# Kernel tuning notes

Hardware: AMD Instinct MI355X
Metric: run time of the kernel (lower is better)

## Reference

```python
import jax, jax.numpy as jnp
import numpy as np

N = 1_000_000   # total points across batch
INC = 128       # channel width (inc)
B = 16          # number of scans in batch
HID = INC // 4  # reduction=4


def setup_inputs() -> dict:
    key = jax.random.key(0)
    k1, k2, k3, k4 = jax.random.split(key, 4)
    feats = jax.random.normal(k1, (N, INC), dtype=jnp.float32)
    batch_idx = jnp.sort(jax.random.randint(k2, (N,), 0, B, dtype=jnp.int32))
    W1 = jax.random.normal(k3, (INC, HID), dtype=jnp.float32) * 0.05
    b1 = jnp.zeros((HID,), dtype=jnp.float32)
    W2 = jax.random.normal(k4, (HID, INC), dtype=jnp.float32) * 0.05
    b2 = jnp.zeros((INC,), dtype=jnp.float32)
    return {"feats": feats, "batch_idx": batch_idx, "W1": W1, "b1": b1, "W2": W2, "b2": b2}


def reference(feats, batch_idx, W1, b1, W2, b2):
    # Segment (per-scan) mean and max over points -> [B, INC].
    counts = jax.ops.segment_sum(jnp.ones((feats.shape[0],), feats.dtype), batch_idx, num_segments=B)
    seg_sum = jax.ops.segment_sum(feats, batch_idx, num_segments=B)
    seg_mean = seg_sum / jnp.maximum(counts, 1.0)[:, None]
    seg_max = jax.ops.segment_max(feats, batch_idx, num_segments=B)
    seg_max = jnp.where(counts[:, None] > 0, seg_max, 0.0)  # guard empty segments

    def mlp(z):
        return jax.nn.relu(z @ W1 + b1) @ W2 + b2

    # sigmoid(MLP(avg) + MLP(max)); pooled values are identical for every
    # point of a segment, so apply MLP on [B, INC] and gather per point.
    gate = jax.nn.sigmoid(mlp(seg_mean) + mlp(seg_max))  # [B, INC]
    return feats * gate[batch_idx]                        # [N, INC]
```

## Files before the change

kernel.cpp:

```cpp
#include <hip/hip_runtime.h>
#include <math.h>

#define INC   128
#define HID   32
#define NSEG  16

typedef float f4v __attribute__((ext_vector_type(4)));

__device__ __forceinline__ float4 ntload4(const float4* p) {
    f4v v = __builtin_nontemporal_load((const f4v*)p);
    return make_float4(v.x, v.y, v.z, v.w);
}
__device__ __forceinline__ void ntstore4(float4* p, float4 f) {
    f4v v = {f.x, f.y, f.z, f.w};
    __builtin_nontemporal_store(v, (f4v*)p);
}

__device__ __forceinline__ unsigned f2ord(float f) {
    unsigned u = __float_as_uint(f);
    return (u & 0x80000000u) ? ~u : (u | 0x80000000u);
}
__device__ __forceinline__ float ord2f(unsigned u) {
    return (u & 0x80000000u) ? __uint_as_float(u & 0x7fffffffu)
                             : __uint_as_float(~u);
}

__device__ __forceinline__ void flush_lds8(int seg, int c8,
                                           const float4& s0, const float4& s1,
                                           const float4& m0, const float4& m1,
                                           float cnt, float* s_sum,
                                           unsigned* s_max, float* s_cnt) {
    int base = seg * INC + c8 * 8;
    atomicAdd(&s_sum[base + 0], s0.x);
    atomicAdd(&s_sum[base + 1], s0.y);
    atomicAdd(&s_sum[base + 2], s0.z);
    atomicAdd(&s_sum[base + 3], s0.w);
    atomicAdd(&s_sum[base + 4], s1.x);
    atomicAdd(&s_sum[base + 5], s1.y);
    atomicAdd(&s_sum[base + 6], s1.z);
    atomicAdd(&s_sum[base + 7], s1.w);
    atomicMax(&s_max[base + 0], f2ord(m0.x));
    atomicMax(&s_max[base + 1], f2ord(m0.y));
    atomicMax(&s_max[base + 2], f2ord(m0.z));
    atomicMax(&s_max[base + 3], f2ord(m0.w));
    atomicMax(&s_max[base + 4], f2ord(m1.x));
    atomicMax(&s_max[base + 5], f2ord(m1.y));
    atomicMax(&s_max[base + 6], f2ord(m1.z));
    atomicMax(&s_max[base + 7], f2ord(m1.w));
    if (c8 == 0) atomicAdd(&s_cnt[seg], cnt);
}

__global__ __launch_bounds__(256) void seg_reduce_kernel(
    const float4* __restrict__ feats4, const int* __restrict__ bidx,
    float* __restrict__ gsum, unsigned* __restrict__ gmax,
    float* __restrict__ gcnt, int nrows)
{
    __shared__ float    s_sum[NSEG * INC];
    __shared__ unsigned s_max[NSEG * INC];
    __shared__ float    s_cnt[NSEG];

    const int tid   = threadIdx.x;
    const int chunk = (nrows + gridDim.x - 1) / gridDim.x;
    const int start = blockIdx.x * chunk;
    if (start >= nrows) return;
    const int end = min(start + chunk, nrows);

    for (int i = tid; i < NSEG * INC; i += 256) { s_sum[i] = 0.f; s_max[i] = 0u; }
    if (tid < NSEG) s_cnt[tid] = 0.f;
    __syncthreads();

    const int c8   = tid & 15;
    const int slot = tid >> 4;
    int    cur = -1;
    float4 s0 = make_float4(0.f, 0.f, 0.f, 0.f), s1 = s0;
    float4 m0 = s0, m1 = s0;
    float  cnt = 0.f;

    for (int r = start + slot; r < end; r += 16) {
        int           seg  = bidx[r];
        const float4* rowp = feats4 + (size_t)r * (INC / 4) + c8 * 2;
        float4        f0   = ntload4(rowp);
        float4        f1   = ntload4(rowp + 1);
        if (seg != cur) {
            if (cur >= 0) flush_lds8(cur, c8, s0, s1, m0, m1, cnt, s_sum, s_max, s_cnt);
            cur = seg; s0 = f0; s1 = f1; m0 = f0; m1 = f1; cnt = 1.f;
        } else {
            s0.x += f0.x; s0.y += f0.y; s0.z += f0.z; s0.w += f0.w;
            s1.x += f1.x; s1.y += f1.y; s1.z += f1.z; s1.w += f1.w;
            m0.x = fmaxf(m0.x, f0.x); m0.y = fmaxf(m0.y, f0.y);
            m0.z = fmaxf(m0.z, f0.z); m0.w = fmaxf(m0.w, f0.w);
            m1.x = fmaxf(m1.x, f1.x); m1.y = fmaxf(m1.y, f1.y);
            m1.z = fmaxf(m1.z, f1.z); m1.w = fmaxf(m1.w, f1.w);
            cnt += 1.f;
        }
    }
    if (cur >= 0) flush_lds8(cur, c8, s0, s1, m0, m1, cnt, s_sum, s_max, s_cnt);
    __syncthreads();

    const int sf  = bidx[start];
    const int sl  = bidx[end - 1];
    const int col = tid & (INC - 1);
    for (int s = sf + (tid >> 7); s <= sl; s += 2) {
        atomicAdd(&gsum[s * INC + col], s_sum[s * INC + col]);
        atomicMax(&gmax[s * INC + col], s_max[s * INC + col]);
        if (col == 0) atomicAdd(&gcnt[s], s_cnt[s]);
    }
}

__global__ __launch_bounds__(256) void mlp_kernel(
    const float* __restrict__ gsum, const unsigned* __restrict__ gmax,
    const float* __restrict__ gcnt,
    const float* __restrict__ W1, const float* __restrict__ b1,
    const float* __restrict__ W2, const float* __restrict__ b2,
    float* __restrict__ gate)
{
    __shared__ float s_mean[NSEG * INC];
    __shared__ float s_max [NSEG * INC];
    __shared__ float s_h   [NSEG * HID];
    __shared__ float s_W1  [INC * HID];
    __shared__ float s_W2  [HID * INC];
    __shared__ float s_b1  [HID];
    __shared__ float s_b2  [INC];
    const int tid = threadIdx.x;

    for (int i = tid; i < INC * HID; i += 256) { s_W1[i] = W1[i]; s_W2[i] = W2[i]; }
    if (tid < HID) s_b1[tid] = b1[tid];
    if (tid < INC) s_b2[tid] = b2[tid];

    for (int i = tid; i < NSEG * INC; i += 256) {
        int   s = i >> 7;
        float c = gcnt[s];
        s_mean[i] = gsum[i] / fmaxf(c, 1.f);
        s_max[i]  = (c > 0.f) ? ord2f(gmax[i]) : 0.f;
    }
    __syncthreads();

    for (int i = tid; i < NSEG * HID; i += 256) {
        int s = i / HID, h = i % HID;
        float am = s_b1[h], ax = s_b1[h];
        for (int c = 0; c < INC; c++) {
            float w = s_W1[c * HID + h];
            am += s_mean[s * INC + c] * w;
            ax += s_max [s * INC + c] * w;
        }
        s_h[i] = fmaxf(am, 0.f) + fmaxf(ax, 0.f);
    }
    __syncthreads();

    for (int i = tid; i < NSEG * INC; i += 256) {
        int s = i >> 7, c = i & (INC - 1);
        float a = 2.f * s_b2[c];
        for (int h = 0; h < HID; h++) a += s_h[s * HID + h] * s_W2[h * INC + c];
        gate[i] = 1.f / (1.f + expf(-a));
    }
}

__global__ __launch_bounds__(256) void apply_kernel(
    const float4* __restrict__ feats4, const int* __restrict__ bidx,
    const float4* __restrict__ gate4, float4* __restrict__ out4, int nrows)
{
    __shared__ float4 s_gate[NSEG * (INC / 4)];
    for (int i = threadIdx.x; i < NSEG * (INC / 4); i += blockDim.x)
        s_gate[i] = gate4[i];
    __syncthreads();

    const int total = nrows * (INC / 4);
    for (int idx = blockIdx.x * blockDim.x + threadIdx.x; idx < total;
         idx += gridDim.x * blockDim.x) {
        int    r   = idx >> 5;
        int    c4  = idx & 31;
        int    seg = bidx[r];
        float4 f   = ntload4(&feats4[idx]);
        float4 g   = s_gate[seg * (INC / 4) + c4];
        ntstore4(&out4[idx],
                 make_float4(f.x * g.x, f.y * g.y, f.z * g.z, f.w * g.w));
    }
}

extern "C" void kernel_launch(void* const* d_in, const int* in_sizes, int n_in,
                              void* d_out, int out_size, void* d_ws, size_t ws_size,
                              hipStream_t stream) {
    const float* feats = (const float*)d_in[0];
    const int*   bidx  = (const int*)d_in[1];
    const float* W1    = (const float*)d_in[2];
    const float* b1    = (const float*)d_in[3];
    const float* W2    = (const float*)d_in[4];
    const float* b2    = (const float*)d_in[5];
    float*       out   = (float*)d_out;
    const int nrows    = in_sizes[1];

    char*     ws   = (char*)d_ws;
    float*    gsum = (float*)(ws);
    unsigned* gmax = (unsigned*)(ws + 8192);
    float*    gcnt = (float*)(ws + 16384);
    float*    gate = (float*)(ws + 16448);

    hipMemsetAsync(d_ws, 0, 16448, stream);

    seg_reduce_kernel<<<2048, 256, 0, stream>>>(
        (const float4*)feats, bidx, gsum, gmax, gcnt, nrows);
    mlp_kernel<<<1, 256, 0, stream>>>(gsum, gmax, gcnt, W1, b1, W2, b2, gate);
    apply_kernel<<<8192, 256, 0, stream>>>(
        (const float4*)feats, bidx, (const float4*)gate, (float4*)out, nrows);
}
```

Baseline: 926.5 us.

## Process segments in groups so reduce and apply reuse feats from cache

Splits the work into four groups of four segments. Each group runs a reduce kernel and then an apply kernel that computes its own gates, so the apply pass rereads a feats slice (about 128MB) that may still sit in the large last-level cache. Nontemporal loads are dropped so the data can stay cached. The separate MLP kernel is folded into each apply block, which recomputes the gate MLP redundantly from global weights. The cost is eight launches instead of three, binary searches, and per-block MLP overhead.

```diff
diff --git a/kernel.cpp b/kernel.cpp
--- a/kernel.cpp
+++ b/kernel.cpp
@@ -1,16 +1,14 @@
 #include <hip/hip_runtime.h>
 #include <math.h>
 
-#define INC   128
-#define HID   32
-#define NSEG  16
+#define INC    128
+#define HID    32
+#define NSEG   16
+#define SPG    4
+#define NGRP   (NSEG / SPG)
+#define NBLK   2048
 
 typedef float f4v __attribute__((ext_vector_type(4)));
-
-__device__ __forceinline__ float4 ntload4(const float4* p) {
-    f4v v = __builtin_nontemporal_load((const f4v*)p);
-    return make_float4(v.x, v.y, v.z, v.w);
-}
 __device__ __forceinline__ void ntstore4(float4* p, float4 f) {
     f4v v = {f.x, f.y, f.z, f.w};
     __builtin_nontemporal_store(v, (f4v*)p);
@@ -25,49 +23,51 @@
                              : __uint_as_float(~u);
 }
 
-__device__ __forceinline__ void flush_lds8(int seg, int c8,
+__device__ __forceinline__ int lower_bound(const int* __restrict__ a, int n, int v) {
+    int lo = 0, hi = n;
+    while (lo < hi) { int m = (lo + hi) >> 1; if (a[m] < v) lo = m + 1; else hi = m; }
+    return lo;
+}
+
+__device__ __forceinline__ void flush_lds8(int sseg, int c8,
                                            const float4& s0, const float4& s1,
                                            const float4& m0, const float4& m1,
                                            float cnt, float* s_sum,
                                            unsigned* s_max, float* s_cnt) {
-    int base = seg * INC + c8 * 8;
-    atomicAdd(&s_sum[base + 0], s0.x);
-    atomicAdd(&s_sum[base + 1], s0.y);
-    atomicAdd(&s_sum[base + 2], s0.z);
-    atomicAdd(&s_sum[base + 3], s0.w);
-    atomicAdd(&s_sum[base + 4], s1.x);
-    atomicAdd(&s_sum[base + 5], s1.y);
-    atomicAdd(&s_sum[base + 6], s1.z);
-    atomicAdd(&s_sum[base + 7], s1.w);
-    atomicMax(&s_max[base + 0], f2ord(m0.x));
-    atomicMax(&s_max[base + 1], f2ord(m0.y));
-    atomicMax(&s_max[base + 2], f2ord(m0.z));
-    atomicMax(&s_max[base + 3], f2ord(m0.w));
-    atomicMax(&s_max[base + 4], f2ord(m1.x));
-    atomicMax(&s_max[base + 5], f2ord(m1.y));
-    atomicMax(&s_max[base + 6], f2ord(m1.z));
-    atomicMax(&s_max[base + 7], f2ord(m1.w));
-    if (c8 == 0) atomicAdd(&s_cnt[seg], cnt);
+    int base = sseg * INC + c8 * 8;
+    atomicAdd(&s_sum[base + 0], s0.x);  atomicAdd(&s_sum[base + 1], s0.y);
+    atomicAdd(&s_sum[base + 2], s0.z);  atomicAdd(&s_sum[base + 3], s0.w);
+    atomicAdd(&s_sum[base + 4], s1.x);  atomicAdd(&s_sum[base + 5], s1.y);
+    atomicAdd(&s_sum[base + 6], s1.z);  atomicAdd(&s_sum[base + 7], s1.w);
+    atomicMax(&s_max[base + 0], f2ord(m0.x));  atomicMax(&s_max[base + 1], f2ord(m0.y));
+    atomicMax(&s_max[base + 2], f2ord(m0.z));  atomicMax(&s_max[base + 3], f2ord(m0.w));
+    atomicMax(&s_max[base + 4], f2ord(m1.x));  atomicMax(&s_max[base + 5], f2ord(m1.y));
+    atomicMax(&s_max[base + 6], f2ord(m1.z));  atomicMax(&s_max[base + 7], f2ord(m1.w));
+    if (c8 == 0) atomicAdd(&s_cnt[sseg], cnt);
 }
 
-__global__ __launch_bounds__(256) void seg_reduce_kernel(
+__global__ __launch_bounds__(256) void seg_reduce_group(
     const float4* __restrict__ feats4, const int* __restrict__ bidx,
     float* __restrict__ gsum, unsigned* __restrict__ gmax,
-    float* __restrict__ gcnt, int nrows)
+    float* __restrict__ gcnt, int nrows, int seg_lo)
 {
-    __shared__ float    s_sum[NSEG * INC];
-    __shared__ unsigned s_max[NSEG * INC];
-    __shared__ float    s_cnt[NSEG];
+    __shared__ float    s_sum[SPG * INC];
+    __shared__ unsigned s_max[SPG * INC];
+    __shared__ float    s_cnt[SPG];
+    __shared__ int      s_bounds[2];
 
-    const int tid   = threadIdx.x;
-    const int chunk = (nrows + gridDim.x - 1) / gridDim.x;
-    const int start = blockIdx.x * chunk;
-    if (start >= nrows) return;
-    const int end = min(start + chunk, nrows);
+    const int tid = threadIdx.x;
+    if (tid < 2) s_bounds[tid] = lower_bound(bidx, nrows, seg_lo + tid * SPG);
+    for (int i = tid; i < SPG * INC; i += 256) { s_sum[i] = 0.f; s_max[i] = 0u; }
+    if (tid < SPG) s_cnt[tid] = 0.f;
+    __syncthreads();
 
-    for (int i = tid; i < NSEG * INC; i += 256) { s_sum[i] = 0.f; s_max[i] = 0u; }
-    if (tid < NSEG) s_cnt[tid] = 0.f;
-    __syncthreads();
+    const int r0 = s_bounds[0], r1 = s_bounds[1];
+    if (r1 <= r0) return;
+    const int chunk = (r1 - r0 + NBLK - 1) / NBLK;
+    const int rs = min(r0 + (int)blockIdx.x * chunk, r1);
+    const int re = min(rs + chunk, r1);
+    if (rs >= re) return;
 
     const int c8   = tid & 15;
     const int slot = tid >> 4;
@@ -76,13 +76,14 @@
     float4 m0 = s0, m1 = s0;
     float  cnt = 0.f;
 
-    for (int r = start + slot; r < end; r += 16) {
+    for (int r = rs + slot; r < re; r += 16) {
         int           seg  = bidx[r];
-        const float4* rowp = feats4 + (size_t)r * (INC / 4) + c8 * 2;
-        float4        f0   = ntload4(rowp);
-        float4        f1   = ntload4(rowp + 1);
+        const float4* rowp = feats4 + (size_t)r * 32 + c8 * 2;
+        float4        f0   = rowp[0];
+        float4        f1   = rowp[1];
         if (seg != cur) {
-            if (cur >= 0) flush_lds8(cur, c8, s0, s1, m0, m1, cnt, s_sum, s_max, s_cnt);
+            if (cur >= 0) flush_lds8(cur - seg_lo, c8, s0, s1, m0, m1, cnt,
+                                     s_sum, s_max, s_cnt);
             cur = seg; s0 = f0; s1 = f1; m0 = f0; m1 = f1; cnt = 1.f;
         } else {
             s0.x += f0.x; s0.y += f0.y; s0.z += f0.z; s0.w += f0.w;
@@ -94,85 +95,76 @@
             cnt += 1.f;
         }
     }
-    if (cur >= 0) flush_lds8(cur, c8, s0, s1, m0, m1, cnt, s_sum, s_max, s_cnt);
+    if (cur >= 0) flush_lds8(cur - seg_lo, c8, s0, s1, m0, m1, cnt,
+                             s_sum, s_max, s_cnt);
     __syncthreads();
 
-    const int sf  = bidx[start];
-    const int sl  = bidx[end - 1];
+    const int sf  = bidx[rs] - seg_lo;
+    const int sl  = bidx[re - 1] - seg_lo;
     const int col = tid & (INC - 1);
     for (int s = sf + (tid >> 7); s <= sl; s += 2) {
-        atomicAdd(&gsum[s * INC + col], s_sum[s * INC + col]);
-        atomicMax(&gmax[s * INC + col], s_max[s * INC + col]);
-        if (col == 0) atomicAdd(&gcnt[s], s_cnt[s]);
+        atomicAdd(&gsum[(seg_lo + s) * INC + col], s_sum[s * INC + col]);
+        atomicMax(&gmax[(seg_lo + s) * INC + col], s_max[s * INC + col]);
+        if (col == 0) atomicAdd(&gcnt[seg_lo + s], s_cnt[s]);
     }
 }
 
-__global__ __launch_bounds__(256) void mlp_kernel(
+__global__ __launch_bounds__(256) void apply_group(
+    const float4* __restrict__ feats4, const int* __restrict__ bidx,
     const float* __restrict__ gsum, const unsigned* __restrict__ gmax,
     const float* __restrict__ gcnt,
     const float* __restrict__ W1, const float* __restrict__ b1,
     const float* __restrict__ W2, const float* __restrict__ b2,
-    float* __restrict__ gate)
+    float4* __restrict__ out4, int nrows, int seg_lo)
 {
-    __shared__ float s_mean[NSEG * INC];
-    __shared__ float s_max [NSEG * INC];
-    __shared__ float s_h   [NSEG * HID];
-    __shared__ float s_W1  [INC * HID];
-    __shared__ float s_W2  [HID * INC];
-    __shared__ float s_b1  [HID];
-    __shared__ float s_b2  [INC];
+    __shared__ float4 s_gate[SPG * (INC / 4)];
+    __shared__ float  s_row[2 * INC];
+    __shared__ float  s_hh[2 * HID];
+    __shared__ int    s_bounds[2];
+
     const int tid = threadIdx.x;
-
-    for (int i = tid; i < INC * HID; i += 256) { s_W1[i] = W1[i]; s_W2[i] = W2[i]; }
-    if (tid < HID) s_b1[tid] = b1[tid];
-    if (tid < INC) s_b2[tid] = b2[tid];
-
-    for (int i = tid; i < NSEG * INC; i += 256) {
-        int   s = i >> 7;
-        float c = gcnt[s];
-        s_mean[i] = gsum[i] / fmaxf(c, 1.f);
-        s_max[i]  = (c > 0.f) ? ord2f(gmax[i]) : 0.f;
-    }
+    if (tid < 2) s_bounds[tid] = lower_bound(bidx, nrows, seg_lo + tid * SPG);
     __syncthreads();
 
-    for (int i = tid; i < NSEG * HID; i += 256) {
-        int s = i / HID, h = i % HID;
-        float am = s_b1[h], ax = s_b1[h];
-        for (int c = 0; c < INC; c++) {
-            float w = s_W1[c * HID + h];
-            am += s_mean[s * INC + c] * w;
-            ax += s_max [s * INC + c] * w;
+    const int r0 = s_bounds[0], r1 = s_bounds[1];
+    if (r1 <= r0) return;
+    const int chunk = (r1 - r0 + NBLK - 1) / NBLK;
+    const int rs = min(r0 + (int)blockIdx.x * chunk, r1);
+    const int re = min(rs + chunk, r1);
+    if (rs >= re) return;
+
+    const int sf = bidx[rs], sl = bidx[re - 1];
+    for (int s = sf; s <= sl; ++s) {
+        if (tid < INC) {
+            float c = gcnt[s];
+            s_row[tid]       = gsum[s * INC + tid] / fmaxf(c, 1.f);
+            s_row[INC + tid] = (c > 0.f) ? ord2f(gmax[s * INC + tid]) : 0.f;
         }
-        s_h[i] = fmaxf(am, 0.f) + fmaxf(ax, 0.f);
+        __syncthreads();
+        if (tid < 2 * HID) {
+            int h = tid & (HID - 1);
+            const float* src = s_row + ((tid < HID) ? 0 : INC);
+            float a = b1[h];
+            for (int c = 0; c < INC; ++c) a += src[c] * W1[c * HID + h];
+            s_hh[tid] = fmaxf(a, 0.f);
+        }
+        __syncthreads();
+        if (tid < INC) {
+            float a = 2.f * b2[tid];
+            for (int h = 0; h < HID; ++h)
+                a += (s_hh[h] + s_hh[HID + h]) * W2[h * INC + tid];
+            ((float*)s_gate)[(s - seg_lo) * INC + tid] = 1.f / (1.f + expf(-a));
+        }
+        __syncthreads();
     }
-    __syncthreads();
 
-    for (int i = tid; i < NSEG * INC; i += 256) {
-        int s = i >> 7, c = i & (INC - 1);
-        float a = 2.f * s_b2[c];
-        for (int h = 0; h < HID; h++) a += s_h[s * HID + h] * s_W2[h * INC + c];
-        gate[i] = 1.f / (1.f + expf(-a));
-    }
-}
-
-__global__ __launch_bounds__(256) void apply_kernel(
-    const float4* __restrict__ feats4, const int* __restrict__ bidx,
-    const float4* __restrict__ gate4, float4* __restrict__ out4, int nrows)
-{
-    __shared__ float4 s_gate[NSEG * (INC / 4)];
-    for (int i = threadIdx.x; i < NSEG * (INC / 4); i += blockDim.x)
-        s_gate[i] = gate4[i];
-    __syncthreads();
-
-    const int total = nrows * (INC / 4);
-    for (int idx = blockIdx.x * blockDim.x + threadIdx.x; idx < total;
-         idx += gridDim.x * blockDim.x) {
-        int    r   = idx >> 5;
-        int    c4  = idx & 31;
-        int    seg = bidx[r];
-        float4 f   = ntload4(&feats4[idx]);
-        float4 g   = s_gate[seg * (INC / 4) + c4];
-        ntstore4(&out4[idx],
+    for (int i = rs * 32 + tid; i < re * 32; i += 256) {
+        int    r   = i >> 5;
+        int    c4  = i & 31;
+        int    sg  = bidx[r] - seg_lo;
+        float4 f   = feats4[(size_t)i];
+        float4 g   = s_gate[sg * 32 + c4];
+        ntstore4(&out4[(size_t)i],
                  make_float4(f.x * g.x, f.y * g.y, f.z * g.z, f.w * g.w));
     }
 }
@@ -180,26 +172,26 @@
 extern "C" void kernel_launch(void* const* d_in, const int* in_sizes, int n_in,
                               void* d_out, int out_size, void* d_ws, size_t ws_size,
                               hipStream_t stream) {
-    const float* feats = (const float*)d_in[0];
-    const int*   bidx  = (const int*)d_in[1];
-    const float* W1    = (const float*)d_in[2];
-    const float* b1    = (const float*)d_in[3];
-    const float* W2    = (const float*)d_in[4];
-    const float* b2    = (const float*)d_in[5];
-    float*       out   = (float*)d_out;
-    const int nrows    = in_sizes[1];
+    const float4* feats4 = (const float4*)d_in[0];
+    const int*    bidx   = (const int*)d_in[1];
+    const float*  W1     = (const float*)d_in[2];
+    const float*  b1     = (const float*)d_in[3];
+    const float*  W2     = (const float*)d_in[4];
+    const float*  b2     = (const float*)d_in[5];
+    float4*       out4   = (float4*)d_out;
+    const int     nrows  = in_sizes[1];
 
     char*     ws   = (char*)d_ws;
     float*    gsum = (float*)(ws);
     unsigned* gmax = (unsigned*)(ws + 8192);
     float*    gcnt = (float*)(ws + 16384);
-    float*    gate = (float*)(ws + 16448);
 
     hipMemsetAsync(d_ws, 0, 16448, stream);
 
-    seg_reduce_kernel<<<2048, 256, 0, stream>>>(
-        (const float4*)feats, bidx, gsum, gmax, gcnt, nrows);
-    mlp_kernel<<<1, 256, 0, stream>>>(gsum, gmax, gcnt, W1, b1, W2, b2, gate);
-    apply_kernel<<<8192, 256, 0, stream>>>(
-        (const float4*)feats, bidx, (const float4*)gate, (float4*)out, nrows);
+    for (int g = 0; g < NGRP; ++g) {
+        seg_reduce_group<<<NBLK, 256, 0, stream>>>(
+            feats4, bidx, gsum, gmax, gcnt, nrows, g * SPG);
+        apply_group<<<NBLK, 256, 0, stream>>>(
+            feats4, bidx, gsum, gmax, gcnt, W1, b1, W2, b2, out4, nrows, g * SPG);
+    }
 }
```

After: 1.118 ms. 1.21x slower.
